# Kernel optimization log

Hardware: AMD Instinct MI355X
Metric: run time of the kernel (lower is better)

Reference implementation:

```python
import jax, jax.numpy as jnp
import numpy as np

V = 50257   # n_unique_words
C = 50257   # n_classes
E = 256     # embed_dim
H = 512     # h_dim
S_IN = 512
S_OUT = 511
START = 1


def setup_inputs() -> dict:
    key = jax.random.key(0)
    ks = jax.random.split(key, 12)
    s = 1.0 / np.sqrt(H)
    u = lambda k, shp: jax.random.uniform(k, shp, jnp.float32, -s, s)
    return {
        "h0": jnp.zeros((1, H), jnp.float32),
        "input_ids": jax.random.randint(ks[0], (1, S_IN), 0, V),
        "output_ids": jax.random.randint(ks[1], (1, S_OUT), 0, V),
        "emb": jax.random.normal(ks[2], (V, E), jnp.float32) * 0.02,
        "enc_wih": u(ks[3], (H, E)),
        "enc_whh": u(ks[4], (H, H)),
        "enc_bih": u(ks[5], (H,)),
        "enc_bhh": u(ks[5], (H,)),
        "dec_wih": u(ks[6], (H, E)),
        "dec_whh": u(ks[7], (H, H)),
        "dec_bih": u(ks[8], (H,)),
        "dec_bhh": u(ks[8], (H,)),
        "fc_w": u(ks[9], (C, H)),
        "fc_b": u(ks[10], (C,)),
    }


def _rnn_cell(x, h, wih, whh, bih, bhh):
    # Elman RNNCell: h' = tanh(x W_ih^T + b_ih + h W_hh^T + b_hh)
    return jnp.tanh(x @ wih.T + bih + h @ whh.T + bhh)


def reference(h0, input_ids, output_ids, emb, enc_wih, enc_whh, enc_bih, enc_bhh,
              dec_wih, dec_whh, dec_bih, dec_bhh, fc_w, fc_b):
    # ---- encode ----
    enc_xs = jnp.swapaxes(emb[input_ids], 0, 1)  # [S_in, 1, E]
    def enc_step(h, x):
        h = _rnn_cell(x, h, enc_wih, enc_whh, enc_bih, enc_bhh)
        return h, None
    hn, _ = jax.lax.scan(enc_step, h0, enc_xs)
    # ---- decode_train ----
    start_emb = emb[jnp.array([START])]          # [1, E]
    h1 = _rnn_cell(start_emb, hn, dec_wih, dec_whh, dec_bih, dec_bhh)
    dec_xs = jnp.swapaxes(emb[output_ids], 0, 1)  # [S_out, 1, E]
    def dec_step(h, x):
        h = _rnn_cell(x, h, dec_wih, dec_whh, dec_bih, dec_bhh)
        return h, h
    _, hs = jax.lax.scan(dec_step, h1, dec_xs)    # [S_out, 1, H]
    pred = jnp.concatenate([h1[None], hs], axis=0)[:, 0, :]  # [S_out+1, H]
    return pred @ fc_w.T + fc_b                   # [S_out+1, C]
```

## Files before the change

kernel.cpp:

```cpp
#include <hip/hip_runtime.h>
#include <hip/hip_fp16.h>

#define EDIM 256
#define HDIM 512
#define CDIM 50257

using half2_t = __attribute__((ext_vector_type(2))) _Float16;
using half8_t = __attribute__((ext_vector_type(8))) _Float16;
using float4_t = __attribute__((ext_vector_type(4))) float;

__device__ __forceinline__ float dot2(uint32_t w, uint32_t h, float acc) {
    return __builtin_amdgcn_fdot2(__builtin_bit_cast(half2_t, w),
                                  __builtin_bit_cast(half2_t, h), acc, false);
}

__device__ __forceinline__ float fast_tanh(float x) {
    float e = __builtin_amdgcn_exp2f(x * 2.8853900817779268f);
    return 1.f - 2.f * __builtin_amdgcn_rcpf(e + 1.f);
}

__global__ void __launch_bounds__(256) pack_whh(const float* __restrict__ whh,
                                                _Float16* __restrict__ wpack) {
    int idx = blockIdx.x * blockDim.x + threadIdx.x;
    int g = idx >> 9, t = idx & 511;
    int jr = g >> 2, i = g & 3;
    int row = ((t >> 4) << 4) + jr;
    int k0 = ((t & 15) << 5) + (i << 3);
    const float* src = whh + row * HDIM + k0;
    uint32_t d[4];
#pragma unroll
    for (int q = 0; q < 4; ++q) {
        half2_t p;
        p[0] = (_Float16)src[2 * q];
        p[1] = (_Float16)src[2 * q + 1];
        d[q] = __builtin_bit_cast(uint32_t, p);
    }
    ((uint4*)wpack)[g * 512 + t] = make_uint4(d[0], d[1], d[2], d[3]);
}

__global__ void __launch_bounds__(256) zker(const int* __restrict__ in_ids,
                                            const int* __restrict__ out_ids,
                                            const float* __restrict__ emb,
                                            const float* __restrict__ enc_wih,
                                            const float* __restrict__ enc_bih,
                                            const float* __restrict__ enc_bhh,
                                            const float* __restrict__ dec_wih,
                                            const float* __restrict__ dec_bih,
                                            const float* __restrict__ dec_bhh,
                                            float* __restrict__ z) {
    int t = blockIdx.x;
    const float *wih, *bih, *bhh;
    int id;
    if (t < 512) {
        wih = enc_wih; bih = enc_bih; bhh = enc_bhh; id = in_ids[t];
    } else {
        wih = dec_wih; bih = dec_bih; bhh = dec_bhh;
        id = (t == 512) ? 1 : out_ids[t - 513];
    }
    __shared__ float x[EDIM];
    x[threadIdx.x] = emb[(long)id * EDIM + threadIdx.x];
    __syncthreads();
#pragma unroll
    for (int rr = 0; rr < 2; ++rr) {
        int r = threadIdx.x + rr * 256;
        const float4* w4 = (const float4*)(wih + r * EDIM);
        float acc = 0.f;
#pragma unroll 8
        for (int k4 = 0; k4 < 64; ++k4) {
            float4 wv = w4[k4];
            acc += wv.x * x[k4 * 4 + 0] + wv.y * x[k4 * 4 + 1] +
                   wv.z * x[k4 * 4 + 2] + wv.w * x[k4 * 4 + 3];
        }
        z[t * HDIM + r] = acc + bih[r] + bhh[r];
    }
}

__global__ void __launch_bounds__(512, 2) scan_ker(
    const _Float16* __restrict__ wpack,
    const float* __restrict__ z,
    const _Float16* __restrict__ h_init,
    _Float16* __restrict__ hs_out,
    _Float16* __restrict__ hfin_out,
    int nsteps) {
    __shared__ uint4 wlds[16 * 512];
    __shared__ uint4 hbuf4[2][64];

    const int tid = threadIdx.x;
    const int c = tid & 15;
    const int g_own = tid >> 3;
    const int hstore = 128 * (g_own & 3) + 8 * (g_own >> 2) + (tid & 7);

    const uint4* wp4 = (const uint4*)wpack;
    uint32_t wreg[192];
#pragma unroll
    for (int g = 0; g < 48; ++g) {
        uint4 v = wp4[g * 512 + tid];
        wreg[g * 4 + 0] = v.x; wreg[g * 4 + 1] = v.y;
        wreg[g * 4 + 2] = v.z; wreg[g * 4 + 3] = v.w;
    }
#pragma unroll
    for (int g = 48; g < 64; ++g) wlds[(g - 48) * 512 + tid] = wp4[g * 512 + tid];

    ((_Float16*)hbuf4[0])[hstore] = h_init ? h_init[tid] : (_Float16)0.f;
    __syncthreads();

    int cur = 0;
    for (int t = 0; t < nsteps; ++t) {
        float zv = z[t * HDIM + tid];
        const uint4* hb = hbuf4[cur];
        float acc[16];
#pragma unroll
        for (int r = 0; r < 16; ++r) acc[r] = 0.f;
#pragma unroll
        for (int i = 0; i < 4; ++i) {
            uint4 hg = hb[i * 16 + c];
#pragma unroll
            for (int jr = 0; jr < 12; ++jr) {
                acc[jr] = dot2(wreg[(jr * 4 + i) * 4 + 0], hg.x, acc[jr]);
                acc[jr] = dot2(wreg[(jr * 4 + i) * 4 + 1], hg.y, acc[jr]);
                acc[jr] = dot2(wreg[(jr * 4 + i) * 4 + 2], hg.z, acc[jr]);
                acc[jr] = dot2(wreg[(jr * 4 + i) * 4 + 3], hg.w, acc[jr]);
            }
#pragma unroll
            for (int js = 0; js < 4; ++js) {
                uint4 w = wlds[(js * 4 + i) * 512 + tid];
                acc[12 + js] = dot2(w.x, hg.x, acc[12 + js]);
                acc[12 + js] = dot2(w.y, hg.y, acc[12 + js]);
                acc[12 + js] = dot2(w.z, hg.z, acc[12 + js]);
                acc[12 + js] = dot2(w.w, hg.w, acc[12 + js]);
            }
        }
        float s, keep;
#define FOLD_DPP(aL, aH, bit, ctrl, dst)                                      \
        s = (c & bit) ? (aL) : (aH);                                          \
        s = __builtin_bit_cast(float, __builtin_amdgcn_mov_dpp(               \
                __builtin_bit_cast(int, s), ctrl, 0xF, 0xF, true));           \
        keep = (c & bit) ? (aH) : (aL);                                       \
        dst = keep + s;
#define FOLD_SWZ(aL, aH, bit, pat, dst)                                       \
        s = (c & bit) ? (aL) : (aH);                                          \
        s = __builtin_bit_cast(float, __builtin_amdgcn_ds_swizzle(            \
                __builtin_bit_cast(int, s), pat));                            \
        keep = (c & bit) ? (aH) : (aL);                                       \
        dst = keep + s;
        float b0, b1, b2, b3, b4, b5, b6, b7, d0, d1, d2, d3, e0, e1, v;
        FOLD_DPP(acc[0],  acc[1],  1, 0xB1, b0)
        FOLD_DPP(acc[2],  acc[3],  1, 0xB1, b1)
        FOLD_DPP(acc[4],  acc[5],  1, 0xB1, b2)
        FOLD_DPP(acc[6],  acc[7],  1, 0xB1, b3)
        FOLD_DPP(acc[8],  acc[9],  1, 0xB1, b4)
        FOLD_DPP(acc[10], acc[11], 1, 0xB1, b5)
        FOLD_DPP(acc[12], acc[13], 1, 0xB1, b6)
        FOLD_DPP(acc[14], acc[15], 1, 0xB1, b7)
        FOLD_DPP(b0, b1, 2, 0x4E, d0)
        FOLD_DPP(b2, b3, 2, 0x4E, d1)
        FOLD_DPP(b4, b5, 2, 0x4E, d2)
        FOLD_DPP(b6, b7, 2, 0x4E, d3)
        FOLD_DPP(d0, d2, 8, 0x128, e0)
        FOLD_DPP(d1, d3, 8, 0x128, e1)
        FOLD_SWZ(e0, e1, 4, 0x101F, v)
#undef FOLD_DPP
#undef FOLD_SWZ
        float hnew = fast_tanh(v + zv);
        _Float16 h16v = (_Float16)hnew;
        ((_Float16*)hbuf4[cur ^ 1])[hstore] = h16v;
        if (hs_out) hs_out[t * HDIM + tid] = h16v;
        if (hfin_out && t == nsteps - 1) hfin_out[tid] = h16v;
        __syncthreads();
        cur ^= 1;
    }
}

__global__ void __launch_bounds__(256) cvt_w16(const float* __restrict__ src,
                                               _Float16* __restrict__ dst, long n) {
    long i = ((long)blockIdx.x * 256 + threadIdx.x) * 8;
    if (i + 8 <= n) {
        const float4* s4 = (const float4*)(src + i);
        float4 a = s4[0], b = s4[1];
        half8_t o;
        o[0] = (_Float16)a.x; o[1] = (_Float16)a.y;
        o[2] = (_Float16)a.z; o[3] = (_Float16)a.w;
        o[4] = (_Float16)b.x; o[5] = (_Float16)b.y;
        o[6] = (_Float16)b.z; o[7] = (_Float16)b.w;
        *(half8_t*)(dst + i) = o;
    }
}

__global__ void __launch_bounds__(256) fc_ker16(const _Float16* __restrict__ A,
                                                const _Float16* __restrict__ Bw,
                                                const float* __restrict__ bias,
                                                float* __restrict__ out) {
    int n0 = blockIdx.x * 128, m0 = blockIdx.y * 128;
    int w = threadIdx.x >> 6, l = threadIdx.x & 63;
    int wm = (w >> 1) * 64, wn = (w & 1) * 64;
    int lr = l & 15, lk = (l >> 4) * 8;

    float4_t acc[4][4];
#pragma unroll
    for (int fm = 0; fm < 4; ++fm)
#pragma unroll
        for (int fn = 0; fn < 4; ++fn) acc[fm][fn] = (float4_t){0.f, 0.f, 0.f, 0.f};

    for (int ks = 0; ks < 512; ks += 32) {
        half8_t a[4], b[4];
#pragma unroll
        for (int f = 0; f < 4; ++f) {
            int m = m0 + wm + f * 16 + lr;
            a[f] = *(const half8_t*)(A + (long)m * 512 + ks + lk);
            int n = n0 + wn + f * 16 + lr;
            if (n < CDIM) {
                b[f] = *(const half8_t*)(Bw + (long)n * 512 + ks + lk);
            } else {
#pragma unroll
                for (int e = 0; e < 8; ++e) b[f][e] = (_Float16)0.f;
            }
        }
#pragma unroll
        for (int fm = 0; fm < 4; ++fm)
#pragma unroll
            for (int fn = 0; fn < 4; ++fn)
                acc[fm][fn] = __builtin_amdgcn_mfma_f32_16x16x32_f16(
                    a[fm], b[fn], acc[fm][fn], 0, 0, 0);
    }
#pragma unroll
    for (int fn = 0; fn < 4; ++fn) {
        int n = n0 + wn + fn * 16 + lr;
        if (n >= CDIM) continue;
        float bv = bias[n];
#pragma unroll
        for (int fm = 0; fm < 4; ++fm) {
#pragma unroll
            for (int q = 0; q < 4; ++q) {
                int m = m0 + wm + fm * 16 + (l >> 4) * 4 + q;
                out[(long)m * CDIM + n] = acc[fm][fn][q] + bv;
            }
        }
    }
}

__global__ void __launch_bounds__(256) fc_ker(const _Float16* __restrict__ A,
                                              const float* __restrict__ Bw,
                                              const float* __restrict__ bias,
                                              float* __restrict__ out) {
    int n0 = blockIdx.x * 128, m0 = blockIdx.y * 128;
    int w = threadIdx.x >> 6, l = threadIdx.x & 63;
    int wm = (w >> 1) * 64, wn = (w & 1) * 64;
    int lr = l & 15, lk = (l >> 4) * 8;

    float4_t acc[4][4];
#pragma unroll
    for (int fm = 0; fm < 4; ++fm)
#pragma unroll
        for (int fn = 0; fn < 4; ++fn) acc[fm][fn] = (float4_t){0.f, 0.f, 0.f, 0.f};

    for (int ks = 0; ks < 512; ks += 32) {
        half8_t a[4], b[4];
#pragma unroll
        for (int f = 0; f < 4; ++f) {
            int m = m0 + wm + f * 16 + lr;
            a[f] = *(const half8_t*)(A + (long)m * 512 + ks + lk);
            int n = n0 + wn + f * 16 + lr;
            half8_t bb;
            if (n < CDIM) {
                const float4* bp4 = (const float4*)(Bw + (long)n * 512 + ks + lk);
                float4 x0 = bp4[0], x1 = bp4[1];
                bb[0] = (_Float16)x0.x; bb[1] = (_Float16)x0.y;
                bb[2] = (_Float16)x0.z; bb[3] = (_Float16)x0.w;
                bb[4] = (_Float16)x1.x; bb[5] = (_Float16)x1.y;
                bb[6] = (_Float16)x1.z; bb[7] = (_Float16)x1.w;
            } else {
#pragma unroll
                for (int e = 0; e < 8; ++e) bb[e] = (_Float16)0.f;
            }
            b[f] = bb;
        }
#pragma unroll
        for (int fm = 0; fm < 4; ++fm)
#pragma unroll
            for (int fn = 0; fn < 4; ++fn)
                acc[fm][fn] = __builtin_amdgcn_mfma_f32_16x16x32_f16(
                    a[fm], b[fn], acc[fm][fn], 0, 0, 0);
    }
#pragma unroll
    for (int fn = 0; fn < 4; ++fn) {
        int n = n0 + wn + fn * 16 + lr;
        if (n >= CDIM) continue;
        float bv = bias[n];
#pragma unroll
        for (int fm = 0; fm < 4; ++fm) {
#pragma unroll
            for (int q = 0; q < 4; ++q) {
                int m = m0 + wm + fm * 16 + (l >> 4) * 4 + q;
                out[(long)m * CDIM + n] = acc[fm][fn][q] + bv;
            }
        }
    }
}

extern "C" void kernel_launch(void* const* d_in, const int* in_sizes, int n_in,
                              void* d_out, int out_size, void* d_ws, size_t ws_size,
                              hipStream_t stream) {
    const int* input_ids  = (const int*)d_in[1];
    const int* output_ids = (const int*)d_in[2];
    const float* emb      = (const float*)d_in[3];
    const float* enc_wih  = (const float*)d_in[4];
    const float* enc_whh  = (const float*)d_in[5];
    const float* enc_bih  = (const float*)d_in[6];
    const float* enc_bhh  = (const float*)d_in[7];
    const float* dec_wih  = (const float*)d_in[8];
    const float* dec_whh  = (const float*)d_in[9];
    const float* dec_bih  = (const float*)d_in[10];
    const float* dec_bhh  = (const float*)d_in[11];
    const float* fc_w     = (const float*)d_in[12];
    const float* fc_b     = (const float*)d_in[13];
    float* out = (float*)d_out;

    char* ws = (char*)d_ws;
    float* z        = (float*)ws;
    _Float16* wpe   = (_Float16*)(ws + (2u << 20));
    _Float16* wpd   = (_Float16*)(ws + (2u << 20) + (512u << 10));
    _Float16* h16   = (_Float16*)(ws + (3u << 20));
    _Float16* hn16  = (_Float16*)(ws + (3u << 20) + (512u << 10));
    _Float16* fcw16 = (_Float16*)(ws + (4u << 20));

    const long fcw_n = (long)CDIM * HDIM;
    bool use_f16_fc = ws_size >= (size_t)(4u << 20) + (size_t)fcw_n * 2;

    pack_whh<<<128, 256, 0, stream>>>(enc_whh, wpe);
    pack_whh<<<128, 256, 0, stream>>>(dec_whh, wpd);
    if (use_f16_fc) {
        int nb = (int)((fcw_n / 8 + 255) / 256);
        cvt_w16<<<nb, 256, 0, stream>>>(fc_w, fcw16, fcw_n);
    }
    zker<<<1024, 256, 0, stream>>>(input_ids, output_ids, emb,
                                   enc_wih, enc_bih, enc_bhh,
                                   dec_wih, dec_bih, dec_bhh, z);
    scan_ker<<<1, 512, 0, stream>>>(wpe, z, nullptr, nullptr, hn16, 512);
    scan_ker<<<1, 512, 0, stream>>>(wpd, z + 512 * HDIM, hn16, h16, nullptr, 512);
    if (use_f16_fc)
        fc_ker16<<<dim3((CDIM + 127) / 128, 4), 256, 0, stream>>>(h16, fcw16, fc_b, out);
    else
        fc_ker<<<dim3((CDIM + 127) / 128, 4), 256, 0, stream>>>(h16, fc_w, fc_b, out);
}
```

Measured before the change: 1.626 ms.

## Use packed fp16 FMA chains with XOR-swizzled weight layout to simplify reduction

The recurrent matvec switches from fp32-accumulating fdot2 to packed half2 FMA chains. The weights are repacked with an XOR-swizzled row mapping so each lane's partial sums reduce through plain DPP add trees, with no per-fold select logic. This cuts instruction count in the serial scan step, at the cost of fp16 accumulation over 32-element chains, which lowers numerical precision.

```diff
diff --git a/kernel.cpp b/kernel.cpp
--- a/kernel.cpp
+++ b/kernel.cpp
@@ -9,9 +9,8 @@
 using half8_t = __attribute__((ext_vector_type(8))) _Float16;
 using float4_t = __attribute__((ext_vector_type(4))) float;
 
-__device__ __forceinline__ float dot2(uint32_t w, uint32_t h, float acc) {
-    return __builtin_amdgcn_fdot2(__builtin_bit_cast(half2_t, w),
-                                  __builtin_bit_cast(half2_t, h), acc, false);
+__device__ __forceinline__ half2_t h2(uint32_t x) {
+    return __builtin_bit_cast(half2_t, x);
 }
 
 __device__ __forceinline__ float fast_tanh(float x) {
@@ -23,9 +22,8 @@
                                                 _Float16* __restrict__ wpack) {
     int idx = blockIdx.x * blockDim.x + threadIdx.x;
     int g = idx >> 9, t = idx & 511;
-    int jr = g >> 2, i = g & 3;
-    int row = ((t >> 4) << 4) + jr;
-    int k0 = ((t & 15) << 5) + (i << 3);
+    int row = ((t >> 4) << 4) + ((g >> 2) ^ (t & 15));
+    int k0 = ((t & 15) << 5) + ((g & 3) << 3);
     const float* src = whh + row * HDIM + k0;
     uint32_t d[4];
 #pragma unroll
@@ -91,13 +89,9 @@
     const int hstore = 128 * (g_own & 3) + 8 * (g_own >> 2) + (tid & 7);
 
     const uint4* wp4 = (const uint4*)wpack;
-    uint32_t wreg[192];
-#pragma unroll
-    for (int g = 0; g < 48; ++g) {
-        uint4 v = wp4[g * 512 + tid];
-        wreg[g * 4 + 0] = v.x; wreg[g * 4 + 1] = v.y;
-        wreg[g * 4 + 2] = v.z; wreg[g * 4 + 3] = v.w;
-    }
+    uint4 wreg4[48];
+#pragma unroll
+    for (int g = 0; g < 48; ++g) wreg4[g] = wp4[g * 512 + tid];
 #pragma unroll
     for (int g = 48; g < 64; ++g) wlds[(g - 48) * 512 + tid] = wp4[g * 512 + tid];
 
@@ -108,60 +102,73 @@
     for (int t = 0; t < nsteps; ++t) {
         float zv = z[t * HDIM + tid];
         const uint4* hb = hbuf4[cur];
-        float acc[16];
-#pragma unroll
-        for (int r = 0; r < 16; ++r) acc[r] = 0.f;
-#pragma unroll
-        for (int i = 0; i < 4; ++i) {
-            uint4 hg = hb[i * 16 + c];
-#pragma unroll
-            for (int jr = 0; jr < 12; ++jr) {
-                acc[jr] = dot2(wreg[(jr * 4 + i) * 4 + 0], hg.x, acc[jr]);
-                acc[jr] = dot2(wreg[(jr * 4 + i) * 4 + 1], hg.y, acc[jr]);
-                acc[jr] = dot2(wreg[(jr * 4 + i) * 4 + 2], hg.z, acc[jr]);
-                acc[jr] = dot2(wreg[(jr * 4 + i) * 4 + 3], hg.w, acc[jr]);
-            }
-#pragma unroll
-            for (int js = 0; js < 4; ++js) {
-                uint4 w = wlds[(js * 4 + i) * 512 + tid];
-                acc[12 + js] = dot2(w.x, hg.x, acc[12 + js]);
-                acc[12 + js] = dot2(w.y, hg.y, acc[12 + js]);
-                acc[12 + js] = dot2(w.z, hg.z, acc[12 + js]);
-                acc[12 + js] = dot2(w.w, hg.w, acc[12 + js]);
-            }
-        }
-        float s, keep;
-#define FOLD_DPP(aL, aH, bit, ctrl, dst)                                      \
-        s = (c & bit) ? (aL) : (aH);                                          \
-        s = __builtin_bit_cast(float, __builtin_amdgcn_mov_dpp(               \
-                __builtin_bit_cast(int, s), ctrl, 0xF, 0xF, true));           \
-        keep = (c & bit) ? (aH) : (aL);                                       \
-        dst = keep + s;
-#define FOLD_SWZ(aL, aH, bit, pat, dst)                                       \
-        s = (c & bit) ? (aL) : (aH);                                          \
-        s = __builtin_bit_cast(float, __builtin_amdgcn_ds_swizzle(            \
-                __builtin_bit_cast(int, s), pat));                            \
-        keep = (c & bit) ? (aH) : (aL);                                       \
-        dst = keep + s;
-        float b0, b1, b2, b3, b4, b5, b6, b7, d0, d1, d2, d3, e0, e1, v;
-        FOLD_DPP(acc[0],  acc[1],  1, 0xB1, b0)
-        FOLD_DPP(acc[2],  acc[3],  1, 0xB1, b1)
-        FOLD_DPP(acc[4],  acc[5],  1, 0xB1, b2)
-        FOLD_DPP(acc[6],  acc[7],  1, 0xB1, b3)
-        FOLD_DPP(acc[8],  acc[9],  1, 0xB1, b4)
-        FOLD_DPP(acc[10], acc[11], 1, 0xB1, b5)
-        FOLD_DPP(acc[12], acc[13], 1, 0xB1, b6)
-        FOLD_DPP(acc[14], acc[15], 1, 0xB1, b7)
-        FOLD_DPP(b0, b1, 2, 0x4E, d0)
-        FOLD_DPP(b2, b3, 2, 0x4E, d1)
-        FOLD_DPP(b4, b5, 2, 0x4E, d2)
-        FOLD_DPP(b6, b7, 2, 0x4E, d3)
-        FOLD_DPP(d0, d2, 8, 0x128, e0)
-        FOLD_DPP(d1, d3, 8, 0x128, e1)
-        FOLD_SWZ(e0, e1, 4, 0x101F, v)
-#undef FOLD_DPP
-#undef FOLD_SWZ
-        float hnew = fast_tanh(v + zv);
+        uint4 hg0 = hb[0 * 16 + c];
+        uint4 hg1 = hb[1 * 16 + c];
+        uint4 hg2 = hb[2 * 16 + c];
+        uint4 hg3 = hb[3 * 16 + c];
+        float f[16];
+
+#define CHAIN(W0, W1, W2, W3, OUT) do {                                       \
+        half2_t _a = h2((W0).x) * h2(hg0.x);                                  \
+        _a = __builtin_elementwise_fma(h2((W0).y), h2(hg0.y), _a);            \
+        _a = __builtin_elementwise_fma(h2((W0).z), h2(hg0.z), _a);            \
+        _a = __builtin_elementwise_fma(h2((W0).w), h2(hg0.w), _a);            \
+        _a = __builtin_elementwise_fma(h2((W1).x), h2(hg1.x), _a);            \
+        _a = __builtin_elementwise_fma(h2((W1).y), h2(hg1.y), _a);            \
+        _a = __builtin_elementwise_fma(h2((W1).z), h2(hg1.z), _a);            \
+        _a = __builtin_elementwise_fma(h2((W1).w), h2(hg1.w), _a);            \
+        half2_t _b = h2((W2).x) * h2(hg2.x);                                  \
+        _b = __builtin_elementwise_fma(h2((W2).y), h2(hg2.y), _b);            \
+        _b = __builtin_elementwise_fma(h2((W2).z), h2(hg2.z), _b);            \
+        _b = __builtin_elementwise_fma(h2((W2).w), h2(hg2.w), _b);            \
+        _b = __builtin_elementwise_fma(h2((W3).x), h2(hg3.x), _b);            \
+        _b = __builtin_elementwise_fma(h2((W3).y), h2(hg3.y), _b);            \
+        _b = __builtin_elementwise_fma(h2((W3).z), h2(hg3.z), _b);            \
+        _b = __builtin_elementwise_fma(h2((W3).w), h2(hg3.w), _b);            \
+        half2_t _m = _a + _b;                                                 \
+        OUT = (float)_m[0] + (float)_m[1]; } while (0)
+
+#pragma unroll
+        for (int s = 0; s < 12; ++s)
+            CHAIN(wreg4[s * 4 + 0], wreg4[s * 4 + 1],
+                  wreg4[s * 4 + 2], wreg4[s * 4 + 3], f[s]);
+#pragma unroll
+        for (int js = 0; js < 4; ++js) {
+            uint4 w0 = wlds[(js * 4 + 0) * 512 + tid];
+            uint4 w1 = wlds[(js * 4 + 1) * 512 + tid];
+            uint4 w2 = wlds[(js * 4 + 2) * 512 + tid];
+            uint4 w3 = wlds[(js * 4 + 3) * 512 + tid];
+            CHAIN(w0, w1, w2, w3, f[12 + js]);
+        }
+#undef CHAIN
+
+#define DPPADD(DST, A, B, CTRL) {                                             \
+        int _x = __builtin_amdgcn_mov_dpp(__builtin_bit_cast(int, (B)),       \
+                                          CTRL, 0xF, 0xF, true);              \
+        DST = (A) + __builtin_bit_cast(float, _x); }
+        float t0, t2, t4, t6, t8, t10, t12, t14;
+        DPPADD(t0,  f[0],  f[1],  0xB1)
+        DPPADD(t2,  f[2],  f[3],  0xB1)
+        DPPADD(t4,  f[4],  f[5],  0xB1)
+        DPPADD(t6,  f[6],  f[7],  0xB1)
+        DPPADD(t8,  f[8],  f[9],  0xB1)
+        DPPADD(t10, f[10], f[11], 0xB1)
+        DPPADD(t12, f[12], f[13], 0xB1)
+        DPPADD(t14, f[14], f[15], 0xB1)
+        float u0, u4, u8, u12;
+        DPPADD(u0,  t0,  t2,  0x4E)
+        DPPADD(u4,  t4,  t6,  0x4E)
+        DPPADD(u8,  t8,  t10, 0x4E)
+        DPPADD(u12, t12, t14, 0x4E)
+        float v0, v4;
+        DPPADD(v0, u0, u8,  0x128)
+        DPPADD(v4, u4, u12, 0x128)
+#undef DPPADD
+        float sw = __builtin_bit_cast(float, __builtin_amdgcn_ds_swizzle(
+                       __builtin_bit_cast(int, v4), 0x101F));
+        float vfin = v0 + sw;
+
+        float hnew = fast_tanh(vfin + zv);
         _Float16 h16v = (_Float16)hnew;
         ((_Float16*)hbuf4[cur ^ 1])[hstore] = h16v;
         if (hs_out) hs_out[t * HDIM + tid] = h16v;
```

New measurement: 1.828 ms. 1.12x slower.
